# Performance work log

Hardware: AMD Instinct MI355X
Metric: run time of the kernel (lower is better)

## Reference

```python
import jax, jax.numpy as jnp
import numpy as np
import math

B, N, D_MODEL = 2, 2048, 512
H, D_HEAD = 8, 64
D_FF = 2048
LN_EPS = 1e-5


def layer_norm(x, g, b):
    mu = jnp.mean(x, axis=-1, keepdims=True)
    var = jnp.mean(jnp.square(x - mu), axis=-1, keepdims=True)
    return (x - mu) * jax.lax.rsqrt(var + LN_EPS) * g + b


def setup_inputs() -> dict:
    key = jax.random.key(0)
    ks = jax.random.split(key, 12)
    s = lambda fan_in: 1.0 / math.sqrt(fan_in)
    inp = {
        "x": jax.random.normal(ks[0], (B, N, D_MODEL), dtype=jnp.float32),
        "mask": jax.random.randint(ks[1], (B, 1, N, N), 0, 2) > 0,
        # attention_pre: Linear(d_model -> 3*H*D_HEAD)
        "W_qkv": jax.random.uniform(ks[2], (D_MODEL, 3 * H * D_HEAD), minval=-s(D_MODEL), maxval=s(D_MODEL)),
        "b_qkv": jnp.zeros((3 * H * D_HEAD,), jnp.float32),
        # project: Linear(H*D_HEAD -> d_model)
        "W_proj": jax.random.uniform(ks[3], (H * D_HEAD, D_MODEL), minval=-s(H * D_HEAD), maxval=s(H * D_HEAD)),
        "b_proj": jnp.zeros((D_MODEL,), jnp.float32),
        "ln1_g": jnp.ones((D_MODEL,), jnp.float32),
        "ln1_b": jnp.zeros((D_MODEL,), jnp.float32),
        # mlp: fc(512->2048, relu), fc(2048->512, relu)  (activation on every layer)
        "W1": jax.random.uniform(ks[4], (D_MODEL, D_FF), minval=-s(D_MODEL), maxval=s(D_MODEL)),
        "b1": jnp.zeros((D_FF,), jnp.float32),
        "W2": jax.random.uniform(ks[5], (D_FF, D_MODEL), minval=-s(D_FF), maxval=s(D_FF)),
        "b2": jnp.zeros((D_MODEL,), jnp.float32),
        "ln2_g": jnp.ones((D_MODEL,), jnp.float32),
        "ln2_b": jnp.zeros((D_MODEL,), jnp.float32),
    }
    return inp


def reference(x, mask, W_qkv, b_qkv, W_proj, b_proj, ln1_g, ln1_b, W1, b1, W2, b2, ln2_g, ln2_b):
    # --- Attention (manual QKV matmul-softmax-matmul) ---
    qkv = x @ W_qkv + b_qkv                      # [B,N,3*H*Dh]
    q, k, v = jnp.split(qkv, 3, axis=2)          # each [B,N,H*Dh]
    def split_heads(t):
        return t.reshape(B, N, H, D_HEAD).transpose(0, 2, 1, 3)  # [B,H,N,Dh]
    q, k, v = split_heads(q), split_heads(k), split_heads(v)
    score = jnp.einsum('bhnd,bhmd->bhnm', q, k) / math.sqrt(D_HEAD)  # [B,H,N,N]
    score = jnp.where(mask, score, -1e9)
    score = jax.nn.softmax(score, axis=-1)
    attn = jnp.einsum('bhnm,bhmd->bhnd', score, v)   # [B,H,N,Dh]
    attn = attn.transpose(0, 2, 1, 3).reshape(B, N, H * D_HEAD)
    a = attn @ W_proj + b_proj                   # [B,N,D_MODEL]
    # --- residual + LN1 ---
    x = layer_norm(x + a, ln1_g, ln1_b)
    # --- MLP (relu after both layers, dropout p=0 = identity) ---
    m = jax.nn.relu(jax.nn.relu(x @ W1 + b1) @ W2 + b2)
    x = layer_norm(x + m, ln2_g, ln2_b)
    return x
```

## Files before the change

### kernel.cpp

```cpp
#include <hip/hip_runtime.h>
#include <math.h>

constexpr int BATCH  = 2;
constexpr int SEQ    = 2048;
constexpr int DMODEL = 512;
constexpr int NH     = 8;
constexpr int DHEAD  = 64;
constexpr int ROWS   = BATCH * SEQ;
constexpr size_t SZ  = (size_t)ROWS * DMODEL;
constexpr int NSPLIT = 4;

typedef __attribute__((ext_vector_type(8))) short bf16x8;
typedef __attribute__((ext_vector_type(4))) float f32x4;

__device__ __forceinline__ ushort f2bf(float f) {
    unsigned u = __float_as_uint(f);
    unsigned r = (u + 0x7FFFu + ((u >> 16) & 1u)) >> 16;
    return (ushort)r;
}
__device__ __forceinline__ float bf2f(ushort u) {
    return __uint_as_float((unsigned)u << 16);
}

__device__ __forceinline__ unsigned cvtpk_bf16(float lo, float hi) {
    unsigned r;
    asm("v_cvt_pk_bf16_f32 %0, %1, %2" : "=v"(r) : "v"(lo), "v"(hi));
    return r;
}

__device__ __forceinline__ void gload_lds16(const void* g, void* l) {
    __builtin_amdgcn_global_load_lds(
        (const __attribute__((address_space(1))) void*)g,
        (__attribute__((address_space(3))) void*)l, 16, 0, 0);
}

__global__ __launch_bounds__(256) void detect_mask_k(
    const uint4* __restrict__ m, int* __restrict__ flag)
{
    const int i = blockIdx.x * 256 + threadIdx.x;
    const uint4 v = m[i];
    unsigned b0 = 0, b1 = 0;
    #pragma unroll
    for (int c = 0; c < 4; ++c) {
        const unsigned u = (&v.x)[c];
        b0 |= (u > 1u) ? 1u : 0u;
        b1 |= (u != 0u && u != 0x3F800000u) ? 1u : 0u;
    }
    const int lane = threadIdx.x & 63;
    if (__any(b0) && lane == 0) atomicOr(flag, 1);
    if (__any(b1) && lane == 0) atomicOr(flag, 2);
}

__global__ __launch_bounds__(256) void prep_all_k(
    const float* __restrict__ x, ushort* __restrict__ xb,
    const float* __restrict__ Wq, const float* __restrict__ Wp,
    const float* __restrict__ W1w, const float* __restrict__ W2w,
    ushort* __restrict__ WqT, ushort* __restrict__ WpT,
    ushort* __restrict__ W1T, ushort* __restrict__ W2T,
    const void* __restrict__ maskp, const int* __restrict__ flagp,
    unsigned long long* __restrict__ bits)
{
    __shared__ ushort T[64][65];
    const int bid = blockIdx.x;
    const int t = threadIdx.x;

    if (bid < 2048) {
        const size_t i = ((size_t)bid * 256 + t) * 4;
        float4 v = *(const float4*)(x + i);
        ushort4 o;
        o.x = f2bf(v.x); o.y = f2bf(v.y); o.z = f2bf(v.z); o.w = f2bf(v.w);
        *(ushort4*)(xb + i) = o;
        return;
    }
    if (bid >= 2816) {
        const int w = (bid - 2816) * 4 + (t >> 6);
        const int lane = t & 63;
        const size_t idx = ((size_t)w << 6) + lane;
        const int f = *flagp;
        bool mv;
        if (!(f & 1))      mv = ((const int*)maskp)[idx] != 0;
        else if (!(f & 2)) mv = ((const float*)maskp)[idx] != 0.f;
        else               mv = ((const unsigned char*)maskp)[idx] != 0;
        unsigned long long bal = __ballot(mv);
        if (lane == 0) bits[w] = bal;
        return;
    }
    const int wb = bid - 2048;
    const float* W; ushort* Wt; int K, N, tix, tiy;
    if (wb < 192)      { W = Wq;  Wt = WqT; K = 512;  N = 1536; tix = wb % 24;        tiy = wb / 24; }
    else if (wb < 256) { W = Wp;  Wt = WpT; K = 512;  N = 512;  tix = (wb-192) % 8;   tiy = (wb-192) / 8; }
    else if (wb < 512) { W = W1w; Wt = W1T; K = 512;  N = 2048; tix = (wb-256) % 32;  tiy = (wb-256) / 32; }
    else               { W = W2w; Wt = W2T; K = 2048; N = 512;  tix = (wb-512) % 8;   tiy = (wb-512) / 8; }
    const int k0 = tiy * 64, n0 = tix * 64;
    const int r = t >> 4, c4 = (t & 15) * 4;
    #pragma unroll
    for (int it = 0; it < 4; ++it) {
        const int row = it*16 + r;
        float4 v = *(const float4*)&W[(size_t)(k0 + row) * N + n0 + c4];
        T[c4+0][row] = f2bf(v.x);
        T[c4+1][row] = f2bf(v.y);
        T[c4+2][row] = f2bf(v.z);
        T[c4+3][row] = f2bf(v.w);
    }
    __syncthreads();
    #pragma unroll
    for (int it = 0; it < 4; ++it) {
        const int row = it*16 + r;
        ushort4 o;
        o.x = T[row][c4+0]; o.y = T[row][c4+1];
        o.z = T[row][c4+2]; o.w = T[row][c4+3];
        *(ushort4*)&Wt[(size_t)(n0 + row) * K + k0 + c4] = o;
    }
}

template<int EPI, int BM, int BN>
__global__ __launch_bounds__(256) void mgemm_k(
    const ushort* __restrict__ A,
    const ushort* __restrict__ Wt,
    const float* __restrict__ bias,
    ushort* __restrict__ Cb,
    ushort* __restrict__ Qo, ushort* __restrict__ Ko, ushort* __restrict__ Vo,
    int M, int N, int K)
{
    constexpr int WM  = BM / 2, WN = BN / 2;
    constexpr int MF  = WM / 16, NF = WN / 16;
    constexpr int APW = BM / 32;
    constexpr int BPW = BN / 32;

    __shared__ ushort As[BM * 64];
    __shared__ ushort Bs[BN * 64];

    const int tid  = threadIdx.x;
    const int wid  = tid >> 6, lane = tid & 63;
    const int lq   = lane & 15, lg = lane >> 4;
    const int wr   = wid >> 1,  wc = wid & 1;
    const int bm   = blockIdx.y * BM, bn = blockIdx.x * BN;

    const int srow0 = lane >> 3;
    const int sch   = lane & 7;

    f32x4 acc[MF][NF] = {};

    for (int k0 = 0; k0 < K; k0 += 64) {
        __syncthreads();
        #pragma unroll
        for (int i = 0; i < APW; ++i) {
            const int seg = wid * APW + i;
            const int row = seg * 8 + srow0;
            const int c16 = sch ^ (row & 7);
            gload_lds16(A + (size_t)(bm + row) * K + k0 + c16 * 8, As + seg * 512);
        }
        #pragma unroll
        for (int i = 0; i < BPW; ++i) {
            const int seg = wid * BPW + i;
            const int row = seg * 8 + srow0;
            const int c16 = sch ^ (row & 7);
            gload_lds16(Wt + (size_t)(bn + row) * K + k0 + c16 * 8, Bs + seg * 512);
        }
        __syncthreads();

        #pragma unroll
        for (int ks = 0; ks < 2; ++ks) {
            bf16x8 af[MF], bfr[NF];
            #pragma unroll
            for (int m = 0; m < MF; ++m) {
                const int row = wr*WM + m*16 + lq;
                const int c16 = (ks*4 + lg) ^ (row & 7);
                af[m] = *(const bf16x8*)&As[row * 64 + c16 * 8];
            }
            #pragma unroll
            for (int n = 0; n < NF; ++n) {
                const int row = wc*WN + n*16 + lq;
                const int c16 = (ks*4 + lg) ^ (row & 7);
                bfr[n] = *(const bf16x8*)&Bs[row * 64 + c16 * 8];
            }
            #pragma unroll
            for (int m = 0; m < MF; ++m)
                #pragma unroll
                for (int n = 0; n < NF; ++n)
                    acc[m][n] = __builtin_amdgcn_mfma_f32_16x16x32_bf16(
                        af[m], bfr[n], acc[m][n], 0, 0, 0);
        }
    }

    #pragma unroll
    for (int m = 0; m < MF; ++m) {
        const int row0 = bm + wr*WM + m*16 + lg*4;
        #pragma unroll
        for (int n = 0; n < NF; ++n) {
            const int col = bn + wc*WN + n*16 + lq;
            const float bv = bias[col];
            float v[4];
            #pragma unroll
            for (int r = 0; r < 4; ++r) {
                v[r] = acc[m][n][r] + bv;
                if (EPI == 1) v[r] = fmaxf(v[r], 0.f);
            }
            if (EPI == 3) {
                const int part = col >> 9, hc = col & 511;
                const int hh = hc >> 6, d0 = hc & 63;
                const int bidx = row0 >> 11, nrow0 = row0 & 2047;
                if (part == 2) {
                    ushort4 pv;
                    pv.x = f2bf(v[0]); pv.y = f2bf(v[1]);
                    pv.z = f2bf(v[2]); pv.w = f2bf(v[3]);
                    *(ushort4*)(Vo + (((size_t)bidx*NH + hh)*DHEAD + d0)*SEQ + nrow0) = pv;
                } else {
                    ushort* dst = (part == 0) ? Qo : Ko;
                    #pragma unroll
                    for (int r = 0; r < 4; ++r)
                        dst[((((size_t)bidx*NH + hh)*SEQ + nrow0 + r) << 6) + d0] = f2bf(v[r]);
                }
            } else {
                #pragma unroll
                for (int r = 0; r < 4; ++r)
                    Cb[(size_t)(row0 + r) * N + col] = f2bf(v[r]);
            }
        }
    }
}

__global__ __launch_bounds__(256, 4) void attn_mfma_k(
    const ushort* __restrict__ Qb, const ushort* __restrict__ Kb,
    const ushort* __restrict__ Vtb, const unsigned long long* __restrict__ mbits,
    ushort* __restrict__ Opart, float2* __restrict__ MLpart)
{
    __shared__ ushort Klds[2][64 * 64];
    __shared__ ushort Vlds[2][64 * 64];
    __shared__ ushort Plds[4][16 * 64];

    const int tid  = threadIdx.x;
    const int wid  = tid >> 6;
    const int lane = tid & 63;
    const int lq   = lane & 15;
    const int lg   = lane >> 4;

    const int raw  = blockIdx.x;
    const int xcd  = raw & 7;
    const int idx  = raw >> 3;
    const int bh   = xcd * 2 + (idx >> 5);
    const int tile = idx & 31;
    const int b    = bh >> 3;
    const int qw   = tile * 64 + wid * 16;
    const int s    = blockIdx.y;
    const int c0   = s * 8, c1 = c0 + 8;

    const ushort* Qg = Qb + ((size_t)bh * SEQ + qw + lq) * DHEAD;
    const bf16x8 qf0 = *(const bf16x8*)(Qg + lg * 8);
    const bf16x8 qf1 = *(const bf16x8*)(Qg + 32 + lg * 8);

    const int srow0 = lane >> 3;
    const int sch   = lane & 7;
    const int gc8   = (sch ^ srow0) * 8;

    const ushort* kgb  = Kb  + (size_t)bh * SEQ * DHEAD
                             + (size_t)(wid*16 + srow0) * DHEAD + gc8;
    const ushort* vgb0 = Vtb + (size_t)bh * DHEAD * SEQ
                             + (size_t)(wid*16 + srow0) * SEQ + gc8;
    const ushort* vgb1 = vgb0 + 8 * SEQ;

    ushort* kd0 = &Klds[0][(wid*2)*512];
    ushort* kd1 = &Klds[1][(wid*2)*512];
    ushort* vd0 = &Vlds[0][(wid*2)*512];
    ushort* vd1 = &Vlds[1][(wid*2)*512];

    int kro[4][2], vro[4][2], pwo[4], pro[2];
    #pragma unroll
    for (int kt = 0; kt < 4; ++kt) {
        kro[kt][0] = ((kt*16 + lq)*64 + ((lg     ^ (lq&7))*8)) * 2;
        kro[kt][1] = ((kt*16 + lq)*64 + (((4+lg) ^ (lq&7))*8)) * 2;
        pwo[kt]    = (wid*1024 + lq*64 + (((kt*2 + (lg>>1)) ^ (lq&7))*8) + (lg&1)*4) * 2;
    }
    #pragma unroll
    for (int kk = 0; kk < 2; ++kk) {
        pro[kk] = (wid*1024 + lq*64 + (((kk*4+lg) ^ (lq&7))*8)) * 2;
        #pragma unroll
        for (int nt = 0; nt < 4; ++nt)
            vro[nt][kk] = ((nt*16 + lq)*64 + (((kk*4+lg) ^ (lq&7))*8)) * 2;
    }
    const char* kbase0 = (const char*)&Klds[0][0];
    const char* kbase1 = (const char*)&Klds[1][0];
    const char* vbase0 = (const char*)&Vlds[0][0];
    const char* vbase1 = (const char*)&Vlds[1][0];
    char*       pbase  = (char*)&Plds[0][0];

    const unsigned long long* mrow = mbits + ((size_t)b * SEQ + qw + lq) * (SEQ / 64);

    f32x4 o[4] = {};
    float mrun = -1e30f, lrun = 0.f;
    const float k2 = 0.125f * 1.44269504f;

    {
        const ushort* kp0  = kgb  + (size_t)c0 * 4096;
        const ushort* vq0  = vgb0 + c0 * 64;
        const ushort* vq1  = vgb1 + c0 * 64;
        gload_lds16(kp0,       kd0);
        gload_lds16(kp0 + 512, kd0 + 512);
        gload_lds16(vq0, vd0);
        gload_lds16(vq1, vd0 + 512);
    }
    const ushort* kp  = kgb  + (size_t)(c0 + 1) * 4096;
    const ushort* vp0 = vgb0 + (c0 + 1) * 64;
    const ushort* vp1 = vgb1 + (c0 + 1) * 64;
    unsigned long long mw_cur = mrow[c0];
    __syncthreads();

#define ATTN_CHUNK(CC, KD, VD, KBASE, VBASE)                                   \
    {                                                                          \
        unsigned long long mw_nxt = 0;                                         \
        if ((CC) + 1 < c1) {                                                   \
            mw_nxt = mrow[(CC) + 1];                                           \
            gload_lds16(kp,       (KD));                                       \
            gload_lds16(kp + 512, (KD) + 512);                                 \
            gload_lds16(vp0, (VD));                                            \
            gload_lds16(vp1, (VD) + 512);                                      \
            kp += 4096; vp0 += 64; vp1 += 64;                                  \
        }                                                                      \
        f32x4 st[4];                                                           \
        __builtin_amdgcn_s_setprio(1);                                         \
        _Pragma("unroll")                                                      \
        for (int kt = 0; kt < 4; ++kt) {                                       \
            bf16x8 kf0 = *(const bf16x8*)((KBASE) + kro[kt][0]);               \
            bf16x8 kf1 = *(const bf16x8*)((KBASE) + kro[kt][1]);               \
            f32x4 a = {};                                                      \
            a = __builtin_amdgcn_mfma_f32_16x16x32_bf16(kf0, qf0, a, 0, 0, 0); \
            a = __builtin_amdgcn_mfma_f32_16x16x32_bf16(kf1, qf1, a, 0, 0, 0); \
            st[kt] = a;                                                        \
        }                                                                      \
        __builtin_amdgcn_s_setprio(0);                                         \
        const unsigned long long mws = mw_cur >> (lg * 4);                     \
        const unsigned mlo = (unsigned)mws, mhi = (unsigned)(mws >> 32);       \
        float sv[16];                                                          \
        _Pragma("unroll")                                                      \
        for (int kt = 0; kt < 4; ++kt) {                                       \
            const unsigned half = (kt & 2) ? mhi : mlo;                        \
            _Pragma("unroll")                                                  \
            for (int r = 0; r < 4; ++r) {                                      \
                const unsigned bit = (half >> ((kt & 1)*16 + r)) & 1u;         \
                sv[kt*4 + r] = bit ? st[kt][r] * k2 : -1e9f;                   \
            }                                                                  \
        }                                                                      \
        float cmax = fmaxf(                                                    \
            fmaxf(fmaxf(fmaxf(sv[0],sv[1]),fmaxf(sv[2],sv[3])),                \
                  fmaxf(fmaxf(sv[4],sv[5]),fmaxf(sv[6],sv[7]))),               \
            fmaxf(fmaxf(fmaxf(sv[8],sv[9]),fmaxf(sv[10],sv[11])),              \
                  fmaxf(fmaxf(sv[12],sv[13]),fmaxf(sv[14],sv[15]))));          \
        cmax = fmaxf(cmax, __shfl_xor(cmax, 16));                              \
        cmax = fmaxf(cmax, __shfl_xor(cmax, 32));                              \
        float mnew = mrun, scale = 1.0f;                                       \
        if (!__all(cmax <= mrun)) {                                            \
            mnew  = fmaxf(mrun, cmax);                                         \
            scale = exp2f(mrun - mnew);                                        \
            float sc[4];                                                       \
            _Pragma("unroll")                                                  \
            for (int r = 0; r < 4; ++r) sc[r] = __shfl(scale, lg*4 + r);       \
            _Pragma("unroll")                                                  \
            for (int nt = 0; nt < 4; ++nt)                                     \
                _Pragma("unroll")                                              \
                for (int r = 0; r < 4; ++r) o[nt][r] *= sc[r];                 \
        }                                                                      \
        float ls[4];                                                           \
        _Pragma("unroll")                                                      \
        for (int kt = 0; kt < 4; ++kt) {                                       \
            const float p0 = exp2f(sv[kt*4+0] - mnew);                         \
            const float p1 = exp2f(sv[kt*4+1] - mnew);                         \
            const float p2 = exp2f(sv[kt*4+2] - mnew);                         \
            const float p3 = exp2f(sv[kt*4+3] - mnew);                         \
            ls[kt] = (p0 + p1) + (p2 + p3);                                    \
            uint2 pk;                                                          \
            pk.x = cvtpk_bf16(p0, p1);                                         \
            pk.y = cvtpk_bf16(p2, p3);                                         \
            *(uint2*)(pbase + pwo[kt]) = pk;                                   \
        }                                                                      \
        float lsum = (ls[0] + ls[1]) + (ls[2] + ls[3]);                        \
        lsum += __shfl_xor(lsum, 16);                                          \
        lsum += __shfl_xor(lsum, 32);                                          \
        lrun = lrun * scale + lsum;                                            \
        mrun = mnew;                                                           \
        __builtin_amdgcn_s_setprio(1);                                         \
        _Pragma("unroll")                                                      \
        for (int kk = 0; kk < 2; ++kk) {                                       \
            bf16x8 pf = *(const bf16x8*)(pbase + pro[kk]);                     \
            _Pragma("unroll")                                                  \
            for (int nt = 0; nt < 4; ++nt) {                                   \
                bf16x8 vf = *(const bf16x8*)((VBASE) + vro[nt][kk]);           \
                o[nt] = __builtin_amdgcn_mfma_f32_16x16x32_bf16(               \
                    pf, vf, o[nt], 0, 0, 0);                                   \
            }                                                                  \
        }                                                                      \
        __builtin_amdgcn_s_setprio(0);                                         \
        __syncthreads();                                                       \
        mw_cur = mw_nxt;                                                       \
    }

    for (int c = c0; c < c1; c += 2) {
        ATTN_CHUNK(c,     kd1, vd1, kbase0, vbase0);
        ATTN_CHUNK(c + 1, kd0, vd0, kbase1, vbase1);
    }
#undef ATTN_CHUNK

    #pragma unroll
    for (int nt = 0; nt < 4; ++nt)
        #pragma unroll
        for (int r = 0; r < 4; ++r) {
            const int qrow = qw + lg*4 + r;
            Opart[(((size_t)s*16 + bh)*SEQ + qrow)*64 + nt*16 + lq] = f2bf(o[nt][r]);
        }
    if (lg == 0) {
        float2 ml; ml.x = mrun; ml.y = lrun;
        MLpart[((size_t)s*16 + bh)*SEQ + qw + lq] = ml;
    }
}

__global__ __launch_bounds__(256) void attn_combine_k(
    const ushort* __restrict__ Op, const float2* __restrict__ ML,
    ushort* __restrict__ attnb)
{
    const int row  = blockIdx.x * 4 + (threadIdx.x >> 6);
    const int lane = threadIdx.x & 63;
    const int bh = row >> 11, q = row & 2047;
    const int b = bh >> 3, h = bh & 7;
    float2 ml[NSPLIT];
    float m = -1e30f;
    #pragma unroll
    for (int s = 0; s < NSPLIT; ++s) {
        ml[s] = ML[(size_t)s*16*SEQ + row];
        m = fmaxf(m, ml[s].x);
    }
    float l = 0.f, o = 0.f;
    #pragma unroll
    for (int s = 0; s < NSPLIT; ++s) {
        const float a = exp2f(ml[s].x - m);
        l += ml[s].y * a;
        o += bf2f(Op[((size_t)s*16*SEQ + row)*64 + lane]) * a;
    }
    attnb[((size_t)(b*SEQ + q))*DMODEL + h*DHEAD + lane] = f2bf(o / l);
}

template<int XBF, int ABF>
__global__ __launch_bounds__(256) void add_ln_k(
    const void* __restrict__ X, const void* __restrict__ Aa,
    const float* __restrict__ gg, const float* __restrict__ bb,
    float* __restrict__ outf, ushort* __restrict__ outb)
{
    const int r = blockIdx.x;
    const int t = threadIdx.x;
    const size_t i2 = (size_t)r * 256 + t;
    float x0, x1;
    if (XBF) {
        ushort2 u = ((const ushort2*)X)[i2];
        x0 = bf2f(u.x); x1 = bf2f(u.y);
    } else {
        float2 f = ((const float2*)X)[i2];
        x0 = f.x; x1 = f.y;
    }
    float a0, a1;
    if (ABF) {
        ushort2 u = ((const ushort2*)Aa)[i2];
        a0 = bf2f(u.x); a1 = bf2f(u.y);
    } else {
        float2 f = ((const float2*)Aa)[i2];
        a0 = f.x; a1 = f.y;
    }
    const float v0 = x0 + a0, v1 = x1 + a1;
    float s  = v0 + v1;
    float ss = v0*v0 + v1*v1;
    #pragma unroll
    for (int off = 32; off > 0; off >>= 1) {
        s  += __shfl_down(s,  off);
        ss += __shfl_down(ss, off);
    }
    __shared__ float ps[4], pss[4];
    const int wid = t >> 6;
    if ((t & 63) == 0) { ps[wid] = s; pss[wid] = ss; }
    __syncthreads();
    const float tot  = ps[0] + ps[1] + ps[2] + ps[3];
    const float tots = pss[0] + pss[1] + pss[2] + pss[3];
    const float mean = tot * (1.0f / DMODEL);
    const float var  = tots * (1.0f / DMODEL) - mean * mean;
    const float rstd = rsqrtf(var + 1e-5f);
    const float2 g2 = ((const float2*)gg)[t];
    const float2 b2 = ((const float2*)bb)[t];
    float2 r2;
    r2.x = (v0 - mean) * rstd * g2.x + b2.x;
    r2.y = (v1 - mean) * rstd * g2.y + b2.y;
    if (outf) ((float2*)outf)[i2] = r2;
    if (outb) {
        ushort2 ob; ob.x = f2bf(r2.x); ob.y = f2bf(r2.y);
        ((ushort2*)outb)[i2] = ob;
    }
}

extern "C" void kernel_launch(void* const* d_in, const int* in_sizes, int n_in,
                              void* d_out, int out_size, void* d_ws, size_t ws_size,
                              hipStream_t stream)
{
    const float* x      = (const float*)d_in[0];
    const void*  mask   = d_in[1];
    const float* W_qkv  = (const float*)d_in[2];
    const float* b_qkv  = (const float*)d_in[3];
    const float* W_proj = (const float*)d_in[4];
    const float* b_proj = (const float*)d_in[5];
    const float* ln1_g  = (const float*)d_in[6];
    const float* ln1_b  = (const float*)d_in[7];
    const float* W1     = (const float*)d_in[8];
    const float* b1     = (const float*)d_in[9];
    const float* W2     = (const float*)d_in[10];
    const float* b2     = (const float*)d_in[11];
    const float* ln2_g  = (const float*)d_in[12];
    const float* ln2_b  = (const float*)d_in[13];

    float* ws = (float*)d_ws;
    ushort* xb    = (ushort*)ws;
    ushort* Qb    = (ushort*)(ws + SZ/2);
    ushort* Kb    = (ushort*)(ws + SZ);
    ushort* Vtb   = (ushort*)(ws + SZ + SZ/2);
    ushort* attnb = (ushort*)(ws + 2*SZ);
    ushort* Opart = (ushort*)(ws + 2*SZ + SZ/2);
    float2* MLp   = (float2*)(ws + 4*SZ + SZ/2);
    ushort* ap    = (ushort*)(ws + 2*SZ + SZ/2);
    ushort* x1b   = (ushort*)(ws + 3*SZ);
    ushort* mbuf  = (ushort*)(ws + 3*SZ + SZ/2);
    ushort* hb    = (ushort*)ws;
    ushort* WqkvT = (ushort*)(ws + 5*SZ);
    ushort* WprojT= (ushort*)(ws + 5*SZ + 393216);
    ushort* W1T   = (ushort*)(ws + 5*SZ + 524288);
    ushort* W2T   = (ushort*)(ws + 5*SZ + 1048576);
    unsigned long long* bits = (unsigned long long*)(ws + 5*SZ + 1572864);
    int*    flag  = (int*)(ws + 5*SZ + 1572864 + 262144);

    float* out = (float*)d_out;

    hipMemsetAsync(flag, 0, 4, stream);
    detect_mask_k<<<64, 256, 0, stream>>>((const uint4*)mask, flag);
    prep_all_k<<<2816 + 32768, 256, 0, stream>>>(
        x, xb, W_qkv, W_proj, W1, W2, WqkvT, WprojT, W1T, W2T,
        mask, flag, bits);

    mgemm_k<3,64,128><<<dim3(12, 64), 256, 0, stream>>>(xb, WqkvT, b_qkv,
        nullptr, Qb, Kb, Vtb, ROWS, 3*DMODEL, DMODEL);
    attn_mfma_k<<<dim3(BATCH*NH*(SEQ/64), NSPLIT), 256, 0, stream>>>(
        Qb, Kb, Vtb, bits, Opart, MLp);
    attn_combine_k<<<BATCH*NH*SEQ/4, 256, 0, stream>>>(Opart, MLp, attnb);
    mgemm_k<4,64,64><<<dim3(8, 64), 256, 0, stream>>>(attnb, WprojT, b_proj,
        ap, nullptr, nullptr, nullptr, ROWS, DMODEL, DMODEL);
    add_ln_k<0,1><<<ROWS, 256, 0, stream>>>(x, ap, ln1_g, ln1_b, nullptr, x1b);
    mgemm_k<1,64,128><<<dim3(16, 64), 256, 0, stream>>>(x1b, W1T, b1,
        hb, nullptr, nullptr, nullptr, ROWS, 2048, DMODEL);
    mgemm_k<1,64,64><<<dim3(8, 64), 256, 0, stream>>>(hb, W2T, b2,
        mbuf, nullptr, nullptr, nullptr, ROWS, DMODEL, 2048);
    add_ln_k<1,1><<<ROWS, 256, 0, stream>>>(x1b, mbuf, ln2_g, ln2_b, out, nullptr);
}
```

Before: 158.4 us.

## Switch attention to 32x32x16 MFMA with register-resident P and lazy rescale

Rewrites the attention kernel to use 32x32x16 bf16 MFMAs, with each wave handling 32 query rows and each block 128 rows, which halves the grid. The softmax scale is folded into Q at load time. P is passed from the score accumulator to the PV MFMA operand through cross-lane shuffles instead of a round trip through LDS, and the running-max rescale is skipped unless the new max exceeds the old one by more than 8 (in log2 units). This is meant to cut LDS traffic and per-chunk overhead, at the cost of more register pressure, fewer blocks and the XCD-aware block remapping being dropped.

```diff
diff --git a/kernel.cpp b/kernel.cpp
--- a/kernel.cpp
+++ b/kernel.cpp
@@ -10,8 +10,9 @@
 constexpr size_t SZ  = (size_t)ROWS * DMODEL;
 constexpr int NSPLIT = 4;
 
-typedef __attribute__((ext_vector_type(8))) short bf16x8;
-typedef __attribute__((ext_vector_type(4))) float f32x4;
+typedef __attribute__((ext_vector_type(8)))  short bf16x8;
+typedef __attribute__((ext_vector_type(4)))  float f32x4;
+typedef __attribute__((ext_vector_type(16))) float f32x16;
 
 __device__ __forceinline__ ushort f2bf(float f) {
     unsigned u = __float_as_uint(f);
@@ -33,6 +34,8 @@
         (const __attribute__((address_space(1))) void*)g,
         (__attribute__((address_space(3))) void*)l, 16, 0, 0);
 }
+
+union u32x4_bf16x8 { unsigned u[4]; bf16x8 v; };
 
 __global__ __launch_bounds__(256) void detect_mask_k(
     const uint4* __restrict__ m, int* __restrict__ flag)
@@ -227,27 +230,38 @@
 {
     __shared__ ushort Klds[2][64 * 64];
     __shared__ ushort Vlds[2][64 * 64];
-    __shared__ ushort Plds[4][16 * 64];
 
     const int tid  = threadIdx.x;
     const int wid  = tid >> 6;
     const int lane = tid & 63;
-    const int lq   = lane & 15;
-    const int lg   = lane >> 4;
-
-    const int raw  = blockIdx.x;
-    const int xcd  = raw & 7;
-    const int idx  = raw >> 3;
-    const int bh   = xcd * 2 + (idx >> 5);
-    const int tile = idx & 31;
+    const int l31  = lane & 31;
+    const int hi   = lane >> 5;
+
+    const int bh   = blockIdx.x & 15;
+    const int tile = blockIdx.x >> 4;
     const int b    = bh >> 3;
-    const int qw   = tile * 64 + wid * 16;
+    const int qw   = tile * 128 + wid * 32;
     const int s    = blockIdx.y;
     const int c0   = s * 8, c1 = c0 + 8;
 
-    const ushort* Qg = Qb + ((size_t)bh * SEQ + qw + lq) * DHEAD;
-    const bf16x8 qf0 = *(const bf16x8*)(Qg + lg * 8);
-    const bf16x8 qf1 = *(const bf16x8*)(Qg + 32 + lg * 8);
+    const float k2 = 0.125f * 1.44269504f;
+
+    bf16x8 qf[4];
+    {
+        const ushort* Qg = Qb + ((size_t)bh * SEQ + qw + l31) * DHEAD;
+        #pragma unroll
+        for (int kd = 0; kd < 4; ++kd) {
+            bf16x8 raw = *(const bf16x8*)(Qg + kd*16 + hi*8);
+            u32x4_bf16x8 cc;
+            #pragma unroll
+            for (int p2 = 0; p2 < 4; ++p2) {
+                const float a = bf2f((ushort)raw[2*p2])   * k2;
+                const float c = bf2f((ushort)raw[2*p2+1]) * k2;
+                cc.u[p2] = cvtpk_bf16(a, c);
+            }
+            qf[kd] = cc.v;
+        }
+    }
 
     const int srow0 = lane >> 3;
     const int sch   = lane & 7;
@@ -264,36 +278,32 @@
     ushort* vd0 = &Vlds[0][(wid*2)*512];
     ushort* vd1 = &Vlds[1][(wid*2)*512];
 
-    int kro[4][2], vro[4][2], pwo[4], pro[2];
-    #pragma unroll
-    for (int kt = 0; kt < 4; ++kt) {
-        kro[kt][0] = ((kt*16 + lq)*64 + ((lg     ^ (lq&7))*8)) * 2;
-        kro[kt][1] = ((kt*16 + lq)*64 + (((4+lg) ^ (lq&7))*8)) * 2;
-        pwo[kt]    = (wid*1024 + lq*64 + (((kt*2 + (lg>>1)) ^ (lq&7))*8) + (lg&1)*4) * 2;
-    }
-    #pragma unroll
-    for (int kk = 0; kk < 2; ++kk) {
-        pro[kk] = (wid*1024 + lq*64 + (((kk*4+lg) ^ (lq&7))*8)) * 2;
+    int kro0[4], kro1[4], vro[4][2];
+    #pragma unroll
+    for (int kd = 0; kd < 4; ++kd) {
+        kro0[kd] = ( (l31)      * 64 + (((kd*2+hi) ^ (lane&7)) * 8) ) * 2;
+        kro1[kd] = ( (32 + l31) * 64 + (((kd*2+hi) ^ (lane&7)) * 8) ) * 2;
+    }
+    #pragma unroll
+    for (int ks = 0; ks < 4; ++ks)
         #pragma unroll
-        for (int nt = 0; nt < 4; ++nt)
-            vro[nt][kk] = ((nt*16 + lq)*64 + (((kk*4+lg) ^ (lq&7))*8)) * 2;
-    }
+        for (int dt = 0; dt < 2; ++dt)
+            vro[ks][dt] = ( (dt*32 + l31) * 64 + (((ks*2+hi) ^ (lane&7)) * 8) ) * 2;
+
     const char* kbase0 = (const char*)&Klds[0][0];
     const char* kbase1 = (const char*)&Klds[1][0];
     const char* vbase0 = (const char*)&Vlds[0][0];
     const char* vbase1 = (const char*)&Vlds[1][0];
-    char*       pbase  = (char*)&Plds[0][0];
-
-    const unsigned long long* mrow = mbits + ((size_t)b * SEQ + qw + lq) * (SEQ / 64);
-
-    f32x4 o[4] = {};
+
+    const unsigned long long* mrow = mbits + ((size_t)b * SEQ + qw + l31) * (SEQ / 64);
+
+    f32x16 o0 = {}, o1 = {};
     float mrun = -1e30f, lrun = 0.f;
-    const float k2 = 0.125f * 1.44269504f;
 
     {
-        const ushort* kp0  = kgb  + (size_t)c0 * 4096;
-        const ushort* vq0  = vgb0 + c0 * 64;
-        const ushort* vq1  = vgb1 + c0 * 64;
+        const ushort* kp0 = kgb  + (size_t)c0 * 4096;
+        const ushort* vq0 = vgb0 + c0 * 64;
+        const ushort* vq1 = vgb1 + c0 * 64;
         gload_lds16(kp0,       kd0);
         gload_lds16(kp0 + 512, kd0 + 512);
         gload_lds16(vq0, vd0);
@@ -316,77 +326,91 @@
             gload_lds16(vp1, (VD) + 512);                                      \
             kp += 4096; vp0 += 64; vp1 += 64;                                  \
         }                                                                      \
-        f32x4 st[4];                                                           \
+        f32x16 st0 = {}, st1 = {};                                             \
         __builtin_amdgcn_s_setprio(1);                                         \
         _Pragma("unroll")                                                      \
-        for (int kt = 0; kt < 4; ++kt) {                                       \
-            bf16x8 kf0 = *(const bf16x8*)((KBASE) + kro[kt][0]);               \
-            bf16x8 kf1 = *(const bf16x8*)((KBASE) + kro[kt][1]);               \
-            f32x4 a = {};                                                      \
-            a = __builtin_amdgcn_mfma_f32_16x16x32_bf16(kf0, qf0, a, 0, 0, 0); \
-            a = __builtin_amdgcn_mfma_f32_16x16x32_bf16(kf1, qf1, a, 0, 0, 0); \
-            st[kt] = a;                                                        \
+        for (int kd = 0; kd < 4; ++kd) {                                       \
+            bf16x8 kf0 = *(const bf16x8*)((KBASE) + kro0[kd]);                 \
+            bf16x8 kf1 = *(const bf16x8*)((KBASE) + kro1[kd]);                 \
+            st0 = __builtin_amdgcn_mfma_f32_32x32x16_bf16(kf0, qf[kd], st0, 0, 0, 0); \
+            st1 = __builtin_amdgcn_mfma_f32_32x32x16_bf16(kf1, qf[kd], st1, 0, 0, 0); \
         }                                                                      \
         __builtin_amdgcn_s_setprio(0);                                         \
-        const unsigned long long mws = mw_cur >> (lg * 4);                     \
-        const unsigned mlo = (unsigned)mws, mhi = (unsigned)(mws >> 32);       \
-        float sv[16];                                                          \
+        const unsigned long long mws = mw_cur >> (hi * 4);                     \
+        const unsigned mlo = (unsigned)mws, mhi2 = (unsigned)(mws >> 32);      \
         _Pragma("unroll")                                                      \
-        for (int kt = 0; kt < 4; ++kt) {                                       \
-            const unsigned half = (kt & 2) ? mhi : mlo;                        \
+        for (int r = 0; r < 16; ++r) {                                         \
+            const int pos = (r & 3) + 8 * (r >> 2);                            \
+            st0[r] = ((mlo  >> pos) & 1u) ? st0[r] : -1e9f;                    \
+            st1[r] = ((mhi2 >> pos) & 1u) ? st1[r] : -1e9f;                    \
+        }                                                                      \
+        float cm0 = fmaxf(fmaxf(fmaxf(st0[0],st0[1]),fmaxf(st0[2],st0[3])),    \
+                          fmaxf(fmaxf(st0[4],st0[5]),fmaxf(st0[6],st0[7])));   \
+        cm0 = fmaxf(cm0, fmaxf(fmaxf(fmaxf(st0[8],st0[9]),fmaxf(st0[10],st0[11])), \
+                               fmaxf(fmaxf(st0[12],st0[13]),fmaxf(st0[14],st0[15])))); \
+        float cm1 = fmaxf(fmaxf(fmaxf(st1[0],st1[1]),fmaxf(st1[2],st1[3])),    \
+                          fmaxf(fmaxf(st1[4],st1[5]),fmaxf(st1[6],st1[7])));   \
+        cm1 = fmaxf(cm1, fmaxf(fmaxf(fmaxf(st1[8],st1[9]),fmaxf(st1[10],st1[11])), \
+                               fmaxf(fmaxf(st1[12],st1[13]),fmaxf(st1[14],st1[15])))); \
+        float cmax = fmaxf(cm0, cm1);                                          \
+        cmax = fmaxf(cmax, __shfl_xor(cmax, 32));                              \
+        if (!__all(cmax <= mrun + 8.0f)) {                                     \
+            const float mnew  = fmaxf(mrun, cmax);                             \
+            const float scale = exp2f(mrun - mnew);                            \
             _Pragma("unroll")                                                  \
-            for (int r = 0; r < 4; ++r) {                                      \
-                const unsigned bit = (half >> ((kt & 1)*16 + r)) & 1u;         \
-                sv[kt*4 + r] = bit ? st[kt][r] * k2 : -1e9f;                   \
+            for (int r = 0; r < 16; ++r) {                                     \
+                const float sc = __shfl(scale, (r&3) + 8*(r>>2) + 4*hi);       \
+                o0[r] *= sc; o1[r] *= sc;                                      \
             }                                                                  \
-        }                                                                      \
-        float cmax = fmaxf(                                                    \
-            fmaxf(fmaxf(fmaxf(sv[0],sv[1]),fmaxf(sv[2],sv[3])),                \
-                  fmaxf(fmaxf(sv[4],sv[5]),fmaxf(sv[6],sv[7]))),               \
-            fmaxf(fmaxf(fmaxf(sv[8],sv[9]),fmaxf(sv[10],sv[11])),              \
-                  fmaxf(fmaxf(sv[12],sv[13]),fmaxf(sv[14],sv[15]))));          \
-        cmax = fmaxf(cmax, __shfl_xor(cmax, 16));                              \
-        cmax = fmaxf(cmax, __shfl_xor(cmax, 32));                              \
-        float mnew = mrun, scale = 1.0f;                                       \
-        if (!__all(cmax <= mrun)) {                                            \
-            mnew  = fmaxf(mrun, cmax);                                         \
-            scale = exp2f(mrun - mnew);                                        \
-            float sc[4];                                                       \
-            _Pragma("unroll")                                                  \
-            for (int r = 0; r < 4; ++r) sc[r] = __shfl(scale, lg*4 + r);       \
-            _Pragma("unroll")                                                  \
-            for (int nt = 0; nt < 4; ++nt)                                     \
-                _Pragma("unroll")                                              \
-                for (int r = 0; r < 4; ++r) o[nt][r] *= sc[r];                 \
-        }                                                                      \
-        float ls[4];                                                           \
+            lrun *= scale;                                                     \
+            mrun = mnew;                                                       \
+        }                                                                      \
+        float lsum = 0.f;                                                      \
         _Pragma("unroll")                                                      \
-        for (int kt = 0; kt < 4; ++kt) {                                       \
-            const float p0 = exp2f(sv[kt*4+0] - mnew);                         \
-            const float p1 = exp2f(sv[kt*4+1] - mnew);                         \
-            const float p2 = exp2f(sv[kt*4+2] - mnew);                         \
-            const float p3 = exp2f(sv[kt*4+3] - mnew);                         \
-            ls[kt] = (p0 + p1) + (p2 + p3);                                    \
-            uint2 pk;                                                          \
-            pk.x = cvtpk_bf16(p0, p1);                                         \
-            pk.y = cvtpk_bf16(p2, p3);                                         \
-            *(uint2*)(pbase + pwo[kt]) = pk;                                   \
-        }                                                                      \
-        float lsum = (ls[0] + ls[1]) + (ls[2] + ls[3]);                        \
-        lsum += __shfl_xor(lsum, 16);                                          \
+        for (int r = 0; r < 16; ++r) {                                         \
+            st0[r] = exp2f(st0[r] - mrun);                                     \
+            st1[r] = exp2f(st1[r] - mrun);                                     \
+            lsum += st0[r] + st1[r];                                           \
+        }                                                                      \
         lsum += __shfl_xor(lsum, 32);                                          \
-        lrun = lrun * scale + lsum;                                            \
-        mrun = mnew;                                                           \
+        lrun += lsum;                                                          \
+        unsigned w0[8], w1[8];                                                 \
+        _Pragma("unroll")                                                      \
+        for (int g = 0; g < 4; ++g) {                                          \
+            w0[2*g]   = cvtpk_bf16(st0[4*g+0], st0[4*g+1]);                    \
+            w0[2*g+1] = cvtpk_bf16(st0[4*g+2], st0[4*g+3]);                    \
+            w1[2*g]   = cvtpk_bf16(st1[4*g+0], st1[4*g+1]);                    \
+            w1[2*g+1] = cvtpk_bf16(st1[4*g+2], st1[4*g+3]);                    \
+        }                                                                      \
+        unsigned rcv0[4], rcv1[4];                                             \
+        _Pragma("unroll")                                                      \
+        for (int i = 0; i < 4; ++i) {                                          \
+            const int i2 = i >> 1, wi = i & 1;                                 \
+            const unsigned s0 = hi ? w0[4*i2+wi] : w0[4*i2+2+wi];              \
+            const unsigned s1 = hi ? w1[4*i2+wi] : w1[4*i2+2+wi];              \
+            rcv0[i] = (unsigned)__shfl_xor((int)s0, 32);                       \
+            rcv1[i] = (unsigned)__shfl_xor((int)s1, 32);                       \
+        }                                                                      \
         __builtin_amdgcn_s_setprio(1);                                         \
         _Pragma("unroll")                                                      \
-        for (int kk = 0; kk < 2; ++kk) {                                       \
-            bf16x8 pf = *(const bf16x8*)(pbase + pro[kk]);                     \
-            _Pragma("unroll")                                                  \
-            for (int nt = 0; nt < 4; ++nt) {                                   \
-                bf16x8 vf = *(const bf16x8*)((VBASE) + vro[nt][kk]);           \
-                o[nt] = __builtin_amdgcn_mfma_f32_16x16x32_bf16(               \
-                    pf, vf, o[nt], 0, 0, 0);                                   \
+        for (int ks = 0; ks < 4; ++ks) {                                       \
+            const int i2 = ks & 1;                                             \
+            u32x4_bf16x8 fw;                                                   \
+            if (ks < 2) {                                                      \
+                fw.u[0] = hi ? rcv0[2*i2+0] : w0[4*i2+0];                      \
+                fw.u[1] = hi ? rcv0[2*i2+1] : w0[4*i2+1];                      \
+                fw.u[2] = hi ? w0[4*i2+2]   : rcv0[2*i2+0];                    \
+                fw.u[3] = hi ? w0[4*i2+3]   : rcv0[2*i2+1];                    \
+            } else {                                                           \
+                fw.u[0] = hi ? rcv1[2*i2+0] : w1[4*i2+0];                      \
+                fw.u[1] = hi ? rcv1[2*i2+1] : w1[4*i2+1];                      \
+                fw.u[2] = hi ? w1[4*i2+2]   : rcv1[2*i2+0];                    \
+                fw.u[3] = hi ? w1[4*i2+3]   : rcv1[2*i2+1];                    \
             }                                                                  \
+            bf16x8 vf0 = *(const bf16x8*)((VBASE) + vro[ks][0]);               \
+            bf16x8 vf1 = *(const bf16x8*)((VBASE) + vro[ks][1]);               \
+            o0 = __builtin_amdgcn_mfma_f32_32x32x16_bf16(fw.v, vf0, o0, 0, 0, 0); \
+            o1 = __builtin_amdgcn_mfma_f32_32x32x16_bf16(fw.v, vf1, o1, 0, 0, 0); \
         }                                                                      \
         __builtin_amdgcn_s_setprio(0);                                         \
         __syncthreads();                                                       \
@@ -400,15 +424,15 @@
 #undef ATTN_CHUNK
 
     #pragma unroll
-    for (int nt = 0; nt < 4; ++nt)
-        #pragma unroll
-        for (int r = 0; r < 4; ++r) {
-            const int qrow = qw + lg*4 + r;
-            Opart[(((size_t)s*16 + bh)*SEQ + qrow)*64 + nt*16 + lq] = f2bf(o[nt][r]);
-        }
-    if (lg == 0) {
+    for (int r = 0; r < 16; ++r) {
+        const int qrow = qw + (r&3) + 8*(r>>2) + 4*hi;
+        const size_t base = (((size_t)s*16 + bh)*SEQ + qrow)*64;
+        Opart[base + l31]      = f2bf(o0[r]);
+        Opart[base + 32 + l31] = f2bf(o1[r]);
+    }
+    if (hi == 0) {
         float2 ml; ml.x = mrun; ml.y = lrun;
-        MLpart[((size_t)s*16 + bh)*SEQ + qw + lq] = ml;
+        MLpart[((size_t)s*16 + bh)*SEQ + qw + l31] = ml;
     }
 }
 
@@ -539,7 +563,7 @@
 
     mgemm_k<3,64,128><<<dim3(12, 64), 256, 0, stream>>>(xb, WqkvT, b_qkv,
         nullptr, Qb, Kb, Vtb, ROWS, 3*DMODEL, DMODEL);
-    attn_mfma_k<<<dim3(BATCH*NH*(SEQ/64), NSPLIT), 256, 0, stream>>>(
+    attn_mfma_k<<<dim3(256, NSPLIT), 256, 0, stream>>>(
         Qb, Kb, Vtb, bits, Opart, MLp);
     attn_combine_k<<<BATCH*NH*SEQ/4, 256, 0, stream>>>(Opart, MLp, attnb);
     mgemm_k<4,64,64><<<dim3(8, 64), 256, 0, stream>>>(attnb, WprojT, b_proj,
```

New measurement: 155.3 us. About the same (-2.0%).
